# Performance work log

Hardware: AMD Instinct MI355X
Metric: run time of the kernel (lower is better)

## Reference

```python
import jax, jax.numpy as jnp
import numpy as np

DIM = 512
HEADS = 8
HEAD_DIM = DIM // HEADS
SCALE = DIM ** (-0.5)  # source uses full dim, not head_dim
LAMBDA_COND = 1.0


def setup_inputs() -> dict:
    key = jax.random.key(0)
    ks = jax.random.split(key, 16)
    b, n, m_a, m_s = 4, 2048, 2048, 256
    s = 0.02
    inp = {
        "x": jax.random.normal(ks[0], (b, n, DIM), jnp.float32),
        "audio_context": jax.random.normal(ks[1], (b, m_a, DIM), jnp.float32),
        "singer_context": jax.random.normal(ks[2], (b, m_s, DIM), jnp.float32),
        "Wq": jax.random.normal(ks[3], (DIM, DIM), jnp.float32) * s,
        "bq": jnp.zeros((DIM,), jnp.float32),
        "Wka": jax.random.normal(ks[4], (DIM, DIM), jnp.float32) * s,
        "bka": jnp.zeros((DIM,), jnp.float32),
        "Wva": jax.random.normal(ks[5], (DIM, DIM), jnp.float32) * s,
        "bva": jnp.zeros((DIM,), jnp.float32),
        "Wks": jax.random.normal(ks[6], (DIM, DIM), jnp.float32) * s,
        "bks": jnp.zeros((DIM,), jnp.float32),
        "Wvs": jax.random.normal(ks[7], (DIM, DIM), jnp.float32) * s,
        "bvs": jnp.zeros((DIM,), jnp.float32),
        "Wp": jax.random.normal(ks[8], (DIM, DIM), jnp.float32) * s,
        "bp": jnp.zeros((DIM,), jnp.float32),
    }
    return inp


def _heads(t):
    b, n, c = t.shape
    return t.reshape(b, n, HEADS, HEAD_DIM).transpose(0, 2, 1, 3)  # (b,h,n,d)


def _attend(q, ctx, Wk, bk, Wv, bv):
    k = _heads(ctx @ Wk.T + bk)
    v = _heads(ctx @ Wv.T + bv)
    attn = jax.nn.softmax(jnp.einsum("bhnd,bhmd->bhnm", q, k) * SCALE, axis=-1)
    o = jnp.einsum("bhnm,bhmd->bhnd", attn, v)
    b, h, n, d = o.shape
    return o.transpose(0, 2, 1, 3).reshape(b, n, h * d)


def reference(x, audio_context, singer_context, Wq, bq, Wka, bka, Wva, bva,
              Wks, bks, Wvs, bvs, Wp, bp):
    q = _heads(x @ Wq.T + bq)
    x_audio = _attend(q, audio_context, Wka, bka, Wva, bva)
    x_singer = _attend(q, singer_context, Wks, bks, Wvs, bvs)
    out = x_audio + LAMBDA_COND * x_singer
    return out @ Wp.T + bp
```

## Files before the change

kernel.cpp:

```cpp
#include <hip/hip_runtime.h>

#define DIM 512
#define NQ 2048
#define MA 2048
#define MS 256
#define QSCALE 0.06375864651f

typedef __attribute__((ext_vector_type(8))) short bf16x8;
typedef __attribute__((ext_vector_type(4))) float f32x4;

__device__ __forceinline__ ushort f2b(float f) {
    uint u = __float_as_uint(f);
    u = (u + 0x7fffu + ((u >> 16) & 1u)) >> 16;
    return (ushort)u;
}

__device__ __forceinline__ void gload16(const ushort* g, ushort* l) {
    __builtin_amdgcn_global_load_lds(
        (const __attribute__((address_space(1))) void*)g,
        (__attribute__((address_space(3))) void*)l, 16, 0, 0);
}

__global__ __launch_bounds__(256) void cast_w6(const float* __restrict__ w0,
                                               const float* __restrict__ w1,
                                               const float* __restrict__ w2,
                                               const float* __restrict__ w3,
                                               const float* __restrict__ w4,
                                               const float* __restrict__ w5,
                                               ushort* __restrict__ out) {
    const float* ws[6] = {w0, w1, w2, w3, w4, w5};
    const float* src = ws[blockIdx.y];
    ushort* dst = out + (size_t)blockIdx.y * 262144;
    int i = blockIdx.x * 256 + threadIdx.x;
    float4 v = ((const float4*)src)[i];
    ushort4 o;
    o.x = f2b(v.x); o.y = f2b(v.y); o.z = f2b(v.z); o.w = f2b(v.w);
    ((ushort4*)dst)[i] = o;
}

__global__ __launch_bounds__(256) void cast_act(const float* __restrict__ x,
                                                const float* __restrict__ ac,
                                                const float* __restrict__ scx,
                                                ushort* __restrict__ xb,
                                                ushort* __restrict__ acb,
                                                ushort* __restrict__ scxb) {
    const float* srcs[3] = {x, ac, scx};
    ushort* dsts[3] = {xb, acb, scxb};
    int n4[3] = {1048576, 1048576, 131072};
    int y = blockIdx.y;
    int i = blockIdx.x * 256 + threadIdx.x;
    if (i >= n4[y]) return;
    float4 v = ((const float4*)srcs[y])[i];
    ushort4 o;
    o.x = f2b(v.x); o.y = f2b(v.y); o.z = f2b(v.z); o.w = f2b(v.w);
    ((ushort4*)dsts[y])[i] = o;
}

template<int OUT_F32, int BIAS_ROW, int SCALEQ>
__global__ __launch_bounds__(256) void gemm64(const ushort* __restrict__ A,
                                              const ushort* __restrict__ B,
                                              const float* __restrict__ bias,
                                              void* __restrict__ outp,
                                              int M, int N, int K,
                                              long sB, long sO) {
    __shared__ ushort At[64 * 32];
    __shared__ ushort Bt[128 * 32];
    int t = threadIdx.x;
    int wv = t >> 6, ln = t & 63, l = ln & 15, g = ln >> 4;
    int row0 = blockIdx.x * 64, col0 = blockIdx.y * 128;
    int srow = t >> 2, sko = (t & 3) * 8;
    const ushort* Bz = B + (size_t)blockIdx.z * sB;
    f32x4 acc[4][2];
#pragma unroll
    for (int i = 0; i < 4; i++)
#pragma unroll
        for (int j = 0; j < 2; j++) acc[i][j] = (f32x4){0, 0, 0, 0};

    for (int k0 = 0; k0 < K; k0 += 32) {
        __syncthreads();
        gload16(A + (size_t)(row0 + srow) * K + k0 + sko, At + srow * 32 + sko);
#pragma unroll
        for (int c = 0; c < 2; c++)
            gload16(Bz + (size_t)(col0 + srow + 64 * c) * K + k0 + sko,
                    Bt + (srow + 64 * c) * 32 + sko);
        __syncthreads();
        bf16x8 ar[4], br[2];
#pragma unroll
        for (int i = 0; i < 4; i++)
            ar[i] = *(const bf16x8*)(At + (i * 16 + l) * 32 + g * 8);
#pragma unroll
        for (int j = 0; j < 2; j++)
            br[j] = *(const bf16x8*)(Bt + (wv * 32 + j * 16 + l) * 32 + g * 8);
#pragma unroll
        for (int i = 0; i < 4; i++)
#pragma unroll
            for (int j = 0; j < 2; j++)
                acc[i][j] = __builtin_amdgcn_mfma_f32_16x16x32_bf16(ar[i], br[j], acc[i][j], 0, 0, 0);
    }
#pragma unroll
    for (int i = 0; i < 4; i++) {
#pragma unroll
        for (int j = 0; j < 2; j++) {
            int row = row0 + i * 16 + g * 4;
            int col = col0 + wv * 32 + j * 16 + l;
#pragma unroll
            for (int r = 0; r < 4; r++) {
                float bv = BIAS_ROW ? bias[row + r] : bias[col];
                float o = acc[i][j][r] + bv;
                if (SCALEQ) o *= QSCALE;
                if (OUT_F32)
                    ((float*)outp + (size_t)blockIdx.z * sO)[(size_t)(row + r) * N + col] = o;
                else
                    ((ushort*)outp + (size_t)blockIdx.z * sO)[(size_t)(row + r) * N + col] = f2b(o);
            }
        }
    }
}

__device__ __forceinline__ void attn_ctx(const ushort* __restrict__ Kp,
                                         const ushort* __restrict__ VTp,
                                         int M, int h,
                                         const bf16x8 (&aq)[2][2],
                                         ushort* __restrict__ Kl,
                                         ushort* __restrict__ Vl,
                                         ushort* __restrict__ Pw,
                                         f32x4 (&acc)[2][4], float (&li)[2][4],
                                         int t) {
    int ln = t & 63, l = ln & 15, g = ln >> 4;
    int sr = t >> 3, sc = (t & 7) * 8;
    const ushort* kg = Kp + (size_t)sr * DIM + h * 64 + sc;
    const ushort* vg = VTp + (size_t)(h * 64 + sr) * M + sc;
    bf16x8 k0 = *(const bf16x8*)kg;
    bf16x8 k1 = *(const bf16x8*)(kg + (size_t)32 * DIM);
    bf16x8 v0 = *(const bf16x8*)vg;
    bf16x8 v1 = *(const bf16x8*)(vg + (size_t)32 * M);
    for (int mt = 0; mt < M; mt += 64) {
        __syncthreads();
        *(bf16x8*)(Kl + sr * 72 + sc) = k0;
        *(bf16x8*)(Kl + (sr + 32) * 72 + sc) = k1;
        *(bf16x8*)(Vl + sr * 72 + sc) = v0;
        *(bf16x8*)(Vl + (sr + 32) * 72 + sc) = v1;
        __syncthreads();
        if (mt + 64 < M) {
            k0 = *(const bf16x8*)(kg + (size_t)(mt + 64) * DIM);
            k1 = *(const bf16x8*)(kg + (size_t)(mt + 96) * DIM);
            v0 = *(const bf16x8*)(vg + (mt + 64));
            v1 = *(const bf16x8*)(vg + (size_t)32 * M + (mt + 64));
        }
#pragma unroll
        for (int tt = 0; tt < 4; tt++) {
            bf16x8 kb0 = *(const bf16x8*)(Kl + (16 * tt + l) * 72 + g * 8);
            bf16x8 kb1 = *(const bf16x8*)(Kl + (16 * tt + l) * 72 + 32 + g * 8);
            f32x4 s0 = {0, 0, 0, 0}, s1 = {0, 0, 0, 0};
            s0 = __builtin_amdgcn_mfma_f32_16x16x32_bf16(aq[0][0], kb0, s0, 0, 0, 0);
            s0 = __builtin_amdgcn_mfma_f32_16x16x32_bf16(aq[0][1], kb1, s0, 0, 0, 0);
            s1 = __builtin_amdgcn_mfma_f32_16x16x32_bf16(aq[1][0], kb0, s1, 0, 0, 0);
            s1 = __builtin_amdgcn_mfma_f32_16x16x32_bf16(aq[1][1], kb1, s1, 0, 0, 0);
#pragma unroll
            for (int r = 0; r < 4; r++) {
                float p0 = exp2f(s0[r]);
                float p1 = exp2f(s1[r]);
                li[0][r] += p0;
                li[1][r] += p1;
                Pw[(g * 4 + r) * 72 + 16 * tt + l] =
                    (ushort)((__float_as_uint(p0) + 0x8000u) >> 16);
                Pw[(16 + g * 4 + r) * 72 + 16 * tt + l] =
                    (ushort)((__float_as_uint(p1) + 0x8000u) >> 16);
            }
        }
        bf16x8 pa00 = *(const bf16x8*)(Pw + l * 72 + g * 8);
        bf16x8 pa01 = *(const bf16x8*)(Pw + l * 72 + 32 + g * 8);
        bf16x8 pa10 = *(const bf16x8*)(Pw + (16 + l) * 72 + g * 8);
        bf16x8 pa11 = *(const bf16x8*)(Pw + (16 + l) * 72 + 32 + g * 8);
#pragma unroll
        for (int c = 0; c < 4; c++) {
            bf16x8 vb0 = *(const bf16x8*)(Vl + (c * 16 + l) * 72 + g * 8);
            bf16x8 vb1 = *(const bf16x8*)(Vl + (c * 16 + l) * 72 + 32 + g * 8);
            acc[0][c] = __builtin_amdgcn_mfma_f32_16x16x32_bf16(pa00, vb0, acc[0][c], 0, 0, 0);
            acc[0][c] = __builtin_amdgcn_mfma_f32_16x16x32_bf16(pa01, vb1, acc[0][c], 0, 0, 0);
            acc[1][c] = __builtin_amdgcn_mfma_f32_16x16x32_bf16(pa10, vb0, acc[1][c], 0, 0, 0);
            acc[1][c] = __builtin_amdgcn_mfma_f32_16x16x32_bf16(pa11, vb1, acc[1][c], 0, 0, 0);
        }
    }
}

__global__ __launch_bounds__(256) void attn_kernel(const ushort* __restrict__ q,
                                                   const ushort* __restrict__ Ka,
                                                   const ushort* __restrict__ VTa,
                                                   const ushort* __restrict__ Ks,
                                                   const ushort* __restrict__ VTs,
                                                   ushort* __restrict__ y) {
    __shared__ ushort Kl[64 * 72];
    __shared__ ushort Vl[64 * 72];
    __shared__ ushort Pl[4 * 32 * 72];
    int t = threadIdx.x;
    int wv = t >> 6, ln = t & 63, l = ln & 15, g = ln >> 4;
    int h = blockIdx.y, bi = blockIdx.z;
    int q0 = blockIdx.x * 128 + wv * 32;
    bf16x8 aq[2][2];
#pragma unroll
    for (int s = 0; s < 2; s++)
#pragma unroll
        for (int kc = 0; kc < 2; kc++)
            aq[s][kc] = *(const bf16x8*)(q + (size_t)(bi * NQ + q0 + 16 * s + l) * DIM +
                                         h * 64 + kc * 32 + g * 8);
    ushort* Pw = Pl + wv * 32 * 72;

    f32x4 acc[2][4];
    float li[2][4];
#pragma unroll
    for (int s = 0; s < 2; s++) {
#pragma unroll
        for (int c = 0; c < 4; c++) acc[s][c] = (f32x4){0, 0, 0, 0};
#pragma unroll
        for (int r = 0; r < 4; r++) li[s][r] = 0.f;
    }
    attn_ctx(Ks + (size_t)bi * MS * DIM, VTs + (size_t)bi * DIM * MS, MS, h,
             aq, Kl, Vl, Pw, acc, li, t);
    float yv[2][4][4];
#pragma unroll
    for (int s = 0; s < 2; s++)
#pragma unroll
        for (int r = 0; r < 4; r++) {
            float v = li[s][r];
            v += __shfl_xor(v, 1); v += __shfl_xor(v, 2);
            v += __shfl_xor(v, 4); v += __shfl_xor(v, 8);
            float inv = 1.f / v;
#pragma unroll
            for (int c = 0; c < 4; c++) yv[s][c][r] = acc[s][c][r] * inv;
        }
#pragma unroll
    for (int s = 0; s < 2; s++) {
#pragma unroll
        for (int c = 0; c < 4; c++) acc[s][c] = (f32x4){0, 0, 0, 0};
#pragma unroll
        for (int r = 0; r < 4; r++) li[s][r] = 0.f;
    }
    attn_ctx(Ka + (size_t)bi * MA * DIM, VTa + (size_t)bi * DIM * MA, MA, h,
             aq, Kl, Vl, Pw, acc, li, t);
#pragma unroll
    for (int s = 0; s < 2; s++)
#pragma unroll
        for (int r = 0; r < 4; r++) {
            float v = li[s][r];
            v += __shfl_xor(v, 1); v += __shfl_xor(v, 2);
            v += __shfl_xor(v, 4); v += __shfl_xor(v, 8);
            float inv = 1.f / v;
#pragma unroll
            for (int c = 0; c < 4; c++) {
                float o = yv[s][c][r] + acc[s][c][r] * inv;
                y[(size_t)(bi * NQ + q0 + 16 * s + g * 4 + r) * DIM +
                  h * 64 + c * 16 + l] = f2b(o);
            }
        }
}

extern "C" void kernel_launch(void* const* d_in, const int* in_sizes, int n_in,
                              void* d_out, int out_size, void* d_ws, size_t ws_size,
                              hipStream_t stream) {
    const float* x   = (const float*)d_in[0];
    const float* ac  = (const float*)d_in[1];
    const float* scx = (const float*)d_in[2];
    const float* Wq  = (const float*)d_in[3];
    const float* bq  = (const float*)d_in[4];
    const float* Wka = (const float*)d_in[5];
    const float* bka = (const float*)d_in[6];
    const float* Wva = (const float*)d_in[7];
    const float* bva = (const float*)d_in[8];
    const float* Wks = (const float*)d_in[9];
    const float* bks = (const float*)d_in[10];
    const float* Wvs = (const float*)d_in[11];
    const float* bvs = (const float*)d_in[12];
    const float* Wp  = (const float*)d_in[13];
    const float* bp  = (const float*)d_in[14];

    ushort* wb   = (ushort*)d_ws;
    ushort* wqb  = wb;
    ushort* wkab = wb + 262144;
    ushort* wvab = wb + 2 * 262144;
    ushort* wksb = wb + 3 * 262144;
    ushort* wvsb = wb + 4 * 262144;
    ushort* wpb  = wb + 5 * 262144;
    ushort* xb   = wb + 6 * 262144;
    ushort* acb  = xb + 4194304;
    ushort* scxb = acb + 4194304;
    ushort* qb   = scxb + 524288;
    ushort* kab  = qb + 4194304;
    ushort* vta  = kab + 4194304;
    ushort* ksb  = vta + 4194304;
    ushort* vts  = ksb + 524288;
    ushort* yb   = xb;

    cast_w6<<<dim3(256, 6), 256, 0, stream>>>(Wq, Wka, Wva, Wks, Wvs, Wp, wb);
    cast_act<<<dim3(4096, 3), 256, 0, stream>>>(x, ac, scx, xb, acb, scxb);

    gemm64<0, 0, 1><<<dim3(128, 4, 1), 256, 0, stream>>>(xb,  wqb,  bq,  qb,  8192, 512, 512, 0, 0);
    gemm64<0, 0, 0><<<dim3(128, 4, 1), 256, 0, stream>>>(acb, wkab, bka, kab, 8192, 512, 512, 0, 0);
    gemm64<0, 1, 0><<<dim3(8, 16, 4),  256, 0, stream>>>(wvab, acb, bva, vta, 512, 2048, 512,
                                                         2048L * 512, 512L * 2048);
    gemm64<0, 0, 0><<<dim3(16, 4, 1),  256, 0, stream>>>(scxb, wksb, bks, ksb, 1024, 512, 512, 0, 0);
    gemm64<0, 1, 0><<<dim3(8, 2, 4),   256, 0, stream>>>(wvsb, scxb, bvs, vts, 512, 256, 512,
                                                         256L * 512, 512L * 256);

    attn_kernel<<<dim3(16, 8, 4), 256, 0, stream>>>(qb, kab, vta, ksb, vts, yb);

    gemm64<1, 0, 0><<<dim3(128, 4, 1), 256, 0, stream>>>(yb, wpb, bp, (float*)d_out,
                                                         8192, 512, 512, 0, 0);
}
```

Measured before the change: 259.6 us.

## Fuse casts and projection GEMMs into single launches; retile attention to 16-row waves

```diff
diff --git a/kernel.cpp b/kernel.cpp
--- a/kernel.cpp
+++ b/kernel.cpp
@@ -21,170 +21,166 @@
         (__attribute__((address_space(3))) void*)l, 16, 0, 0);
 }
 
-__global__ __launch_bounds__(256) void cast_w6(const float* __restrict__ w0,
-                                               const float* __restrict__ w1,
-                                               const float* __restrict__ w2,
-                                               const float* __restrict__ w3,
-                                               const float* __restrict__ w4,
-                                               const float* __restrict__ w5,
-                                               ushort* __restrict__ out) {
-    const float* ws[6] = {w0, w1, w2, w3, w4, w5};
-    const float* src = ws[blockIdx.y];
-    ushort* dst = out + (size_t)blockIdx.y * 262144;
-    int i = blockIdx.x * 256 + threadIdx.x;
-    float4 v = ((const float4*)src)[i];
-    ushort4 o;
-    o.x = f2b(v.x); o.y = f2b(v.y); o.z = f2b(v.z); o.w = f2b(v.w);
-    ((ushort4*)dst)[i] = o;
-}
-
-__global__ __launch_bounds__(256) void cast_act(const float* __restrict__ x,
+__global__ __launch_bounds__(256) void cast_all(const float* __restrict__ w0,
+                                                const float* __restrict__ w1,
+                                                const float* __restrict__ w2,
+                                                const float* __restrict__ w3,
+                                                const float* __restrict__ w4,
+                                                const float* __restrict__ w5,
+                                                const float* __restrict__ x,
                                                 const float* __restrict__ ac,
                                                 const float* __restrict__ scx,
-                                                ushort* __restrict__ xb,
-                                                ushort* __restrict__ acb,
-                                                ushort* __restrict__ scxb) {
-    const float* srcs[3] = {x, ac, scx};
-    ushort* dsts[3] = {xb, acb, scxb};
-    int n4[3] = {1048576, 1048576, 131072};
-    int y = blockIdx.y;
+                                                ushort* __restrict__ dst) {
     int i = blockIdx.x * 256 + threadIdx.x;
-    if (i >= n4[y]) return;
-    float4 v = ((const float4*)srcs[y])[i];
-    ushort4 o;
-    o.x = f2b(v.x); o.y = f2b(v.y); o.z = f2b(v.z); o.w = f2b(v.w);
-    ((ushort4*)dsts[y])[i] = o;
-}
-
-template<int OUT_F32, int BIAS_ROW, int SCALEQ>
-__global__ __launch_bounds__(256) void gemm64(const ushort* __restrict__ A,
-                                              const ushort* __restrict__ B,
-                                              const float* __restrict__ bias,
-                                              void* __restrict__ outp,
-                                              int M, int N, int K,
-                                              long sB, long sO) {
-    __shared__ ushort At[64 * 32];
+    const float* s;
+    int o;
+    if (i < 393216) {
+        int w = i >> 16;
+        s = w < 3 ? (w == 0 ? w0 : (w == 1 ? w1 : w2))
+                  : (w == 3 ? w3 : (w == 4 ? w4 : w5));
+        o = i & 65535;
+    } else if (i < 1441792) { s = x;   o = i - 393216; }
+    else if (i < 2490368)   { s = ac;  o = i - 1441792; }
+    else                    { s = scx; o = i - 2490368; }
+    float4 v = ((const float4*)s)[o];
+    ushort4 u;
+    u.x = f2b(v.x); u.y = f2b(v.y); u.z = f2b(v.z); u.w = f2b(v.w);
+    ((ushort4*)dst)[i] = u;
+}
+
+struct GD {
+    const ushort* A; const ushort* B; const float* bias; void* out;
+    long sB, sO;
+    int N, bx, by, blk0, biasrow, scaleq, outf32, pad;
+};
+
+__global__ __launch_bounds__(256) void gemm_fused(GD d0, GD d1, GD d2, GD d3, GD d4) {
+    __shared__ ushort At[128 * 32];
     __shared__ ushort Bt[128 * 32];
+    GD d = d0;
+    int bid = blockIdx.x;
+    if (bid >= d1.blk0) d = d1;
+    if (bid >= d2.blk0) d = d2;
+    if (bid >= d3.blk0) d = d3;
+    if (bid >= d4.blk0) d = d4;
+    int local = bid - d.blk0;
+    int x = local % d.bx;
+    int rem = local / d.bx;
+    int y = rem % d.by;
+    int z = rem / d.by;
+
     int t = threadIdx.x;
     int wv = t >> 6, ln = t & 63, l = ln & 15, g = ln >> 4;
-    int row0 = blockIdx.x * 64, col0 = blockIdx.y * 128;
-    int srow = t >> 2, sko = (t & 3) * 8;
-    const ushort* Bz = B + (size_t)blockIdx.z * sB;
-    f32x4 acc[4][2];
+    int wrow = wv & 1, wcol = wv >> 1;
+    int row0 = x * 128, col0 = y * 128;
+    int srow = t >> 2;
+    int slot = (t & 3) * 8;
+    int sko = ((t ^ srow) & 3) * 8;
+    int kc8 = ((g ^ (l & 3)) & 3) * 8;
+    const ushort* Ab = d.A;
+    const ushort* Bb = d.B + (size_t)z * d.sB;
+    int N = d.N;
+
+    f32x4 acc[4][4];
 #pragma unroll
     for (int i = 0; i < 4; i++)
 #pragma unroll
-        for (int j = 0; j < 2; j++) acc[i][j] = (f32x4){0, 0, 0, 0};
-
-    for (int k0 = 0; k0 < K; k0 += 32) {
-        __syncthreads();
-        gload16(A + (size_t)(row0 + srow) * K + k0 + sko, At + srow * 32 + sko);
-#pragma unroll
-        for (int c = 0; c < 2; c++)
-            gload16(Bz + (size_t)(col0 + srow + 64 * c) * K + k0 + sko,
-                    Bt + (srow + 64 * c) * 32 + sko);
-        __syncthreads();
-        bf16x8 ar[4], br[2];
+        for (int j = 0; j < 4; j++) acc[i][j] = (f32x4){0, 0, 0, 0};
+
+    for (int k0 = 0; k0 < 512; k0 += 32) {
+        __syncthreads();
+#pragma unroll
+        for (int c = 0; c < 2; c++) {
+            gload16(Ab + (size_t)(row0 + srow + 64 * c) * 512 + k0 + sko,
+                    At + (srow + 64 * c) * 32 + slot);
+            gload16(Bb + (size_t)(col0 + srow + 64 * c) * 512 + k0 + sko,
+                    Bt + (srow + 64 * c) * 32 + slot);
+        }
+        __syncthreads();
+        bf16x8 ar[4], br[4];
 #pragma unroll
         for (int i = 0; i < 4; i++)
-            ar[i] = *(const bf16x8*)(At + (i * 16 + l) * 32 + g * 8);
-#pragma unroll
-        for (int j = 0; j < 2; j++)
-            br[j] = *(const bf16x8*)(Bt + (wv * 32 + j * 16 + l) * 32 + g * 8);
+            ar[i] = *(const bf16x8*)(At + (wrow * 64 + i * 16 + l) * 32 + kc8);
+#pragma unroll
+        for (int j = 0; j < 4; j++)
+            br[j] = *(const bf16x8*)(Bt + (wcol * 64 + j * 16 + l) * 32 + kc8);
 #pragma unroll
         for (int i = 0; i < 4; i++)
 #pragma unroll
-            for (int j = 0; j < 2; j++)
+            for (int j = 0; j < 4; j++)
                 acc[i][j] = __builtin_amdgcn_mfma_f32_16x16x32_bf16(ar[i], br[j], acc[i][j], 0, 0, 0);
     }
 #pragma unroll
     for (int i = 0; i < 4; i++) {
 #pragma unroll
-        for (int j = 0; j < 2; j++) {
-            int row = row0 + i * 16 + g * 4;
-            int col = col0 + wv * 32 + j * 16 + l;
+        for (int j = 0; j < 4; j++) {
+            int row = row0 + wrow * 64 + i * 16 + g * 4;
+            int col = col0 + wcol * 64 + j * 16 + l;
 #pragma unroll
             for (int r = 0; r < 4; r++) {
-                float bv = BIAS_ROW ? bias[row + r] : bias[col];
+                float bv = d.biasrow ? d.bias[row + r] : d.bias[col];
                 float o = acc[i][j][r] + bv;
-                if (SCALEQ) o *= QSCALE;
-                if (OUT_F32)
-                    ((float*)outp + (size_t)blockIdx.z * sO)[(size_t)(row + r) * N + col] = o;
+                if (d.scaleq) o *= QSCALE;
+                if (d.outf32)
+                    ((float*)d.out + (size_t)z * d.sO)[(size_t)(row + r) * N + col] = o;
                 else
-                    ((ushort*)outp + (size_t)blockIdx.z * sO)[(size_t)(row + r) * N + col] = f2b(o);
+                    ((ushort*)d.out + (size_t)z * d.sO)[(size_t)(row + r) * N + col] = f2b(o);
             }
         }
     }
 }
 
-__device__ __forceinline__ void attn_ctx(const ushort* __restrict__ Kp,
-                                         const ushort* __restrict__ VTp,
-                                         int M, int h,
-                                         const bf16x8 (&aq)[2][2],
+__device__ __forceinline__ void attn_ctx(const ushort* __restrict__ kg,
+                                         const ushort* __restrict__ vg,
+                                         int M, const bf16x8 (&aq)[2],
                                          ushort* __restrict__ Kl,
                                          ushort* __restrict__ Vl,
                                          ushort* __restrict__ Pw,
-                                         f32x4 (&acc)[2][4], float (&li)[2][4],
-                                         int t) {
-    int ln = t & 63, l = ln & 15, g = ln >> 4;
-    int sr = t >> 3, sc = (t & 7) * 8;
-    const ushort* kg = Kp + (size_t)sr * DIM + h * 64 + sc;
-    const ushort* vg = VTp + (size_t)(h * 64 + sr) * M + sc;
-    bf16x8 k0 = *(const bf16x8*)kg;
-    bf16x8 k1 = *(const bf16x8*)(kg + (size_t)32 * DIM);
-    bf16x8 v0 = *(const bf16x8*)vg;
-    bf16x8 v1 = *(const bf16x8*)(vg + (size_t)32 * M);
+                                         f32x4 (&acc)[4], float& li,
+                                         int l, int g, int sr, int sc) {
+    bf16x8 k = *(const bf16x8*)kg;
+    bf16x8 v = *(const bf16x8*)vg;
     for (int mt = 0; mt < M; mt += 64) {
         __syncthreads();
-        *(bf16x8*)(Kl + sr * 72 + sc) = k0;
-        *(bf16x8*)(Kl + (sr + 32) * 72 + sc) = k1;
-        *(bf16x8*)(Vl + sr * 72 + sc) = v0;
-        *(bf16x8*)(Vl + (sr + 32) * 72 + sc) = v1;
+        *(bf16x8*)(Kl + sr * 72 + sc) = k;
+        *(bf16x8*)(Vl + sr * 72 + sc) = v;
         __syncthreads();
         if (mt + 64 < M) {
-            k0 = *(const bf16x8*)(kg + (size_t)(mt + 64) * DIM);
-            k1 = *(const bf16x8*)(kg + (size_t)(mt + 96) * DIM);
-            v0 = *(const bf16x8*)(vg + (mt + 64));
-            v1 = *(const bf16x8*)(vg + (size_t)32 * M + (mt + 64));
+            k = *(const bf16x8*)(kg + (size_t)(mt + 64) * DIM);
+            v = *(const bf16x8*)(vg + (mt + 64));
         }
 #pragma unroll
         for (int tt = 0; tt < 4; tt++) {
             bf16x8 kb0 = *(const bf16x8*)(Kl + (16 * tt + l) * 72 + g * 8);
             bf16x8 kb1 = *(const bf16x8*)(Kl + (16 * tt + l) * 72 + 32 + g * 8);
-            f32x4 s0 = {0, 0, 0, 0}, s1 = {0, 0, 0, 0};
-            s0 = __builtin_amdgcn_mfma_f32_16x16x32_bf16(aq[0][0], kb0, s0, 0, 0, 0);
-            s0 = __builtin_amdgcn_mfma_f32_16x16x32_bf16(aq[0][1], kb1, s0, 0, 0, 0);
-            s1 = __builtin_amdgcn_mfma_f32_16x16x32_bf16(aq[1][0], kb0, s1, 0, 0, 0);
-            s1 = __builtin_amdgcn_mfma_f32_16x16x32_bf16(aq[1][1], kb1, s1, 0, 0, 0);
-#pragma unroll
-            for (int r = 0; r < 4; r++) {
-                float p0 = exp2f(s0[r]);
-                float p1 = exp2f(s1[r]);
-                li[0][r] += p0;
-                li[1][r] += p1;
-                Pw[(g * 4 + r) * 72 + 16 * tt + l] =
-                    (ushort)((__float_as_uint(p0) + 0x8000u) >> 16);
-                Pw[(16 + g * 4 + r) * 72 + 16 * tt + l] =
-                    (ushort)((__float_as_uint(p1) + 0x8000u) >> 16);
-            }
-        }
-        bf16x8 pa00 = *(const bf16x8*)(Pw + l * 72 + g * 8);
-        bf16x8 pa01 = *(const bf16x8*)(Pw + l * 72 + 32 + g * 8);
-        bf16x8 pa10 = *(const bf16x8*)(Pw + (16 + l) * 72 + g * 8);
-        bf16x8 pa11 = *(const bf16x8*)(Pw + (16 + l) * 72 + 32 + g * 8);
+            f32x4 s = {0, 0, 0, 0};
+            s = __builtin_amdgcn_mfma_f32_16x16x32_bf16(kb0, aq[0], s, 0, 0, 0);
+            s = __builtin_amdgcn_mfma_f32_16x16x32_bf16(kb1, aq[1], s, 0, 0, 0);
+            float p0 = exp2f(s[0]), p1 = exp2f(s[1]);
+            float p2 = exp2f(s[2]), p3 = exp2f(s[3]);
+            li += (p0 + p1) + (p2 + p3);
+            uint u0 = (__float_as_uint(p0) + 0x8000u) >> 16;
+            uint u1 = (__float_as_uint(p1) + 0x8000u) >> 16;
+            uint u2 = (__float_as_uint(p2) + 0x8000u) >> 16;
+            uint u3 = (__float_as_uint(p3) + 0x8000u) >> 16;
+            uint2 pw;
+            pw.x = u0 | (u1 << 16);
+            pw.y = u2 | (u3 << 16);
+            *(uint2*)(Pw + l * 72 + 16 * tt + g * 4) = pw;
+        }
+        bf16x8 pa0 = *(const bf16x8*)(Pw + l * 72 + g * 8);
+        bf16x8 pa1 = *(const bf16x8*)(Pw + l * 72 + 32 + g * 8);
 #pragma unroll
         for (int c = 0; c < 4; c++) {
             bf16x8 vb0 = *(const bf16x8*)(Vl + (c * 16 + l) * 72 + g * 8);
             bf16x8 vb1 = *(const bf16x8*)(Vl + (c * 16 + l) * 72 + 32 + g * 8);
-            acc[0][c] = __builtin_amdgcn_mfma_f32_16x16x32_bf16(pa00, vb0, acc[0][c], 0, 0, 0);
-            acc[0][c] = __builtin_amdgcn_mfma_f32_16x16x32_bf16(pa01, vb1, acc[0][c], 0, 0, 0);
-            acc[1][c] = __builtin_amdgcn_mfma_f32_16x16x32_bf16(pa10, vb0, acc[1][c], 0, 0, 0);
-            acc[1][c] = __builtin_amdgcn_mfma_f32_16x16x32_bf16(pa11, vb1, acc[1][c], 0, 0, 0);
-        }
-    }
-}
-
-__global__ __launch_bounds__(256) void attn_kernel(const ushort* __restrict__ q,
+            acc[c] = __builtin_amdgcn_mfma_f32_16x16x32_bf16(pa0, vb0, acc[c], 0, 0, 0);
+            acc[c] = __builtin_amdgcn_mfma_f32_16x16x32_bf16(pa1, vb1, acc[c], 0, 0, 0);
+        }
+    }
+}
+
+__global__ __launch_bounds__(512) void attn_kernel(const ushort* __restrict__ q,
                                                    const ushort* __restrict__ Ka,
                                                    const ushort* __restrict__ VTa,
                                                    const ushort* __restrict__ Ks,
@@ -192,66 +188,56 @@
                                                    ushort* __restrict__ y) {
     __shared__ ushort Kl[64 * 72];
     __shared__ ushort Vl[64 * 72];
-    __shared__ ushort Pl[4 * 32 * 72];
+    __shared__ ushort Pl[8 * 16 * 72];
     int t = threadIdx.x;
     int wv = t >> 6, ln = t & 63, l = ln & 15, g = ln >> 4;
     int h = blockIdx.y, bi = blockIdx.z;
-    int q0 = blockIdx.x * 128 + wv * 32;
-    bf16x8 aq[2][2];
-#pragma unroll
-    for (int s = 0; s < 2; s++)
-#pragma unroll
-        for (int kc = 0; kc < 2; kc++)
-            aq[s][kc] = *(const bf16x8*)(q + (size_t)(bi * NQ + q0 + 16 * s + l) * DIM +
-                                         h * 64 + kc * 32 + g * 8);
-    ushort* Pw = Pl + wv * 32 * 72;
-
-    f32x4 acc[2][4];
-    float li[2][4];
-#pragma unroll
-    for (int s = 0; s < 2; s++) {
-#pragma unroll
-        for (int c = 0; c < 4; c++) acc[s][c] = (f32x4){0, 0, 0, 0};
-#pragma unroll
-        for (int r = 0; r < 4; r++) li[s][r] = 0.f;
-    }
-    attn_ctx(Ks + (size_t)bi * MS * DIM, VTs + (size_t)bi * DIM * MS, MS, h,
-             aq, Kl, Vl, Pw, acc, li, t);
-    float yv[2][4][4];
-#pragma unroll
-    for (int s = 0; s < 2; s++)
+    int q0 = blockIdx.x * 128 + wv * 16;
+    bf16x8 aq[2];
+    aq[0] = *(const bf16x8*)(q + (size_t)(bi * NQ + q0 + l) * DIM + h * 64 + g * 8);
+    aq[1] = *(const bf16x8*)(q + (size_t)(bi * NQ + q0 + l) * DIM + h * 64 + 32 + g * 8);
+    int sr = t >> 3, sc = (t & 7) * 8;
+    ushort* Pw = Pl + wv * 16 * 72;
+
+    f32x4 acc[4];
+    float li = 0.f;
+#pragma unroll
+    for (int c = 0; c < 4; c++) acc[c] = (f32x4){0, 0, 0, 0};
+
+    {
+        const ushort* kg = Ks + (size_t)bi * MS * DIM + (size_t)sr * DIM + h * 64 + sc;
+        const ushort* vg = VTs + (size_t)bi * DIM * MS + (size_t)(h * 64 + sr) * MS + sc;
+        attn_ctx(kg, vg, MS, aq, Kl, Vl, Pw, acc, li, l, g, sr, sc);
+    }
+    li += __shfl_xor(li, 16);
+    li += __shfl_xor(li, 32);
+    float yv[4][4];
+    float inv[4];
+#pragma unroll
+    for (int r = 0; r < 4; r++) inv[r] = 1.f / __shfl(li, g * 4 + r);
+#pragma unroll
+    for (int c = 0; c < 4; c++)
+#pragma unroll
+        for (int r = 0; r < 4; r++) yv[c][r] = acc[c][r] * inv[r];
+
+#pragma unroll
+    for (int c = 0; c < 4; c++) acc[c] = (f32x4){0, 0, 0, 0};
+    li = 0.f;
+    {
+        const ushort* kg = Ka + (size_t)bi * MA * DIM + (size_t)sr * DIM + h * 64 + sc;
+        const ushort* vg = VTa + (size_t)bi * DIM * MA + (size_t)(h * 64 + sr) * MA + sc;
+        attn_ctx(kg, vg, MA, aq, Kl, Vl, Pw, acc, li, l, g, sr, sc);
+    }
+    li += __shfl_xor(li, 16);
+    li += __shfl_xor(li, 32);
+#pragma unroll
+    for (int r = 0; r < 4; r++) inv[r] = 1.f / __shfl(li, g * 4 + r);
+#pragma unroll
+    for (int c = 0; c < 4; c++)
 #pragma unroll
         for (int r = 0; r < 4; r++) {
-            float v = li[s][r];
-            v += __shfl_xor(v, 1); v += __shfl_xor(v, 2);
-            v += __shfl_xor(v, 4); v += __shfl_xor(v, 8);
-            float inv = 1.f / v;
-#pragma unroll
-            for (int c = 0; c < 4; c++) yv[s][c][r] = acc[s][c][r] * inv;
-        }
-#pragma unroll
-    for (int s = 0; s < 2; s++) {
-#pragma unroll
-        for (int c = 0; c < 4; c++) acc[s][c] = (f32x4){0, 0, 0, 0};
-#pragma unroll
-        for (int r = 0; r < 4; r++) li[s][r] = 0.f;
-    }
-    attn_ctx(Ka + (size_t)bi * MA * DIM, VTa + (size_t)bi * DIM * MA, MA, h,
-             aq, Kl, Vl, Pw, acc, li, t);
-#pragma unroll
-    for (int s = 0; s < 2; s++)
-#pragma unroll
-        for (int r = 0; r < 4; r++) {
-            float v = li[s][r];
-            v += __shfl_xor(v, 1); v += __shfl_xor(v, 2);
-            v += __shfl_xor(v, 4); v += __shfl_xor(v, 8);
-            float inv = 1.f / v;
-#pragma unroll
-            for (int c = 0; c < 4; c++) {
-                float o = yv[s][c][r] + acc[s][c][r] * inv;
-                y[(size_t)(bi * NQ + q0 + 16 * s + g * 4 + r) * DIM +
-                  h * 64 + c * 16 + l] = f2b(o);
-            }
+            float o = yv[c][r] + acc[c][r] * inv[r];
+            y[(size_t)(bi * NQ + q0 + g * 4 + r) * DIM + h * 64 + c * 16 + l] = f2b(o);
         }
 }
 
@@ -291,19 +277,18 @@
     ushort* vts  = ksb + 524288;
     ushort* yb   = xb;
 
-    cast_w6<<<dim3(256, 6), 256, 0, stream>>>(Wq, Wka, Wva, Wks, Wvs, Wp, wb);
-    cast_act<<<dim3(4096, 3), 256, 0, stream>>>(x, ac, scx, xb, acb, scxb);
-
-    gemm64<0, 0, 1><<<dim3(128, 4, 1), 256, 0, stream>>>(xb,  wqb,  bq,  qb,  8192, 512, 512, 0, 0);
-    gemm64<0, 0, 0><<<dim3(128, 4, 1), 256, 0, stream>>>(acb, wkab, bka, kab, 8192, 512, 512, 0, 0);
-    gemm64<0, 1, 0><<<dim3(8, 16, 4),  256, 0, stream>>>(wvab, acb, bva, vta, 512, 2048, 512,
-                                                         2048L * 512, 512L * 2048);
-    gemm64<0, 0, 0><<<dim3(16, 4, 1),  256, 0, stream>>>(scxb, wksb, bks, ksb, 1024, 512, 512, 0, 0);
-    gemm64<0, 1, 0><<<dim3(8, 2, 4),   256, 0, stream>>>(wvsb, scxb, bvs, vts, 512, 256, 512,
-                                                         256L * 512, 512L * 256);
-
-    attn_kernel<<<dim3(16, 8, 4), 256, 0, stream>>>(qb, kab, vta, ksb, vts, yb);
-
-    gemm64<1, 0, 0><<<dim3(128, 4, 1), 256, 0, stream>>>(yb, wpb, bp, (float*)d_out,
-                                                         8192, 512, 512, 0, 0);
-}
+    cast_all<<<10240, 256, 0, stream>>>(Wq, Wka, Wva, Wks, Wvs, Wp, x, ac, scx, wb);
+
+    GD gq   = {xb,   wqb,  bq,  qb,  0, 0,               512,  64, 4,  0,   0, 1, 0, 0};
+    GD gka  = {acb,  wkab, bka, kab, 0, 0,               512,  64, 4,  256, 0, 0, 0, 0};
+    GD gvta = {wvab, acb,  bva, vta, 2048L * 512, 512L * 2048, 2048, 4, 16, 512, 1, 0, 0, 0};
+    GD gks  = {scxb, wksb, bks, ksb, 0, 0,               512,  8,  4,  768, 0, 0, 0, 0};
+    GD gvts = {wvsb, scxb, bvs, vts, 256L * 512, 512L * 256,   256,  4,  2,  800, 1, 0, 0, 0};
+    gemm_fused<<<832, 256, 0, stream>>>(gq, gka, gvta, gks, gvts);
+
+    attn_kernel<<<dim3(16, 8, 4), 512, 0, stream>>>(qb, kab, vta, ksb, vts, yb);
+
+    GD gpr = {yb, wpb, bp, d_out, 0, 0, 512, 64, 4, 0, 0, 0, 1, 0};
+    GD gnv = {nullptr, nullptr, nullptr, nullptr, 0, 0, 0, 1, 1, 1 << 30, 0, 0, 0, 0};
+    gemm_fused<<<256, 256, 0, stream>>>(gpr, gnv, gnv, gnv, gnv);
+}
```

Result: faster. 246.1 us (-5.2%).
